# Performance work log

Hardware: AMD Instinct MI355X
Metric: run time of the kernel (lower is better)

The kernel has to match this reference:

```python
import jax, jax.numpy as jnp
import numpy as np

N_NODES = 50000
N_EDGES = 800000
N_NODE_DICT = 10000
N_EDGE_DICT = 100
EMB = 128
HID = 32
HEADS = 4
SLOPE = 0.2
LN_EPS = 1e-5


def layer_norm(x, gamma, beta):
    mu = jnp.mean(x, axis=-1, keepdims=True)
    var = jnp.mean(jnp.square(x - mu), axis=-1, keepdims=True)
    return (x - mu) * jax.lax.rsqrt(var + LN_EPS) * gamma + beta


def setup_inputs() -> dict:
    key = jax.random.key(0)
    ks = jax.random.split(key, 10)
    D = HID * HEADS
    inp = {
        "node_features": jax.random.randint(ks[0], (N_NODES,), 0, N_NODE_DICT),
        "edge_features": jax.random.randint(ks[1], (N_EDGES,), 0, N_EDGE_DICT),
        "edge_index": jax.random.randint(ks[2], (2, N_EDGES), 0, N_NODES),
        "node_emb": jax.random.normal(ks[3], (N_NODE_DICT, EMB), jnp.float32),
        "edge_emb": jax.random.normal(ks[4], (N_EDGE_DICT, EMB), jnp.float32),
        "w_W": jax.random.normal(ks[5], (EMB, D), jnp.float32) / np.sqrt(EMB),
        "w_b": jnp.zeros((D,), jnp.float32),
        "ew_W": jax.random.normal(ks[6], (EMB, D), jnp.float32) / np.sqrt(EMB),
        "ew_b": jnp.zeros((D,), jnp.float32),
        "attn": jax.random.normal(ks[7], (HEADS, 3 * HID), jnp.float32) * 0.1,
        "ln_gamma": jnp.ones((D,), jnp.float32),
        "ln_beta": jnp.zeros((D,), jnp.float32),
    }
    return inp


def reference(node_features, edge_features, edge_index, node_emb, edge_emb,
              w_W, w_b, ew_W, ew_b, attn, ln_gamma, ln_beta):
    # embedding lookups
    nf = node_emb[node_features]                       # [N, EMB]
    ef = edge_emb[edge_features]                       # [E, EMB]
    # linear projections -> [*, heads, hid]
    h = (nf @ w_W + w_b).reshape(-1, HEADS, HID)       # [N, H, F]
    eh = (ef @ ew_W + ew_b).reshape(-1, HEADS, HID)    # [E, H, F]
    tgt = edge_index[0]
    src = edge_index[1]
    # attn = [a_i || a_j || a_e]; dot with concat == sum of per-part dots
    a_i, a_j, a_e = attn[:, :HID], attn[:, HID:2 * HID], attn[:, 2 * HID:]
    s_i = jnp.einsum('nhf,hf->nh', h, a_i)             # [N, H]
    s_j = jnp.einsum('nhf,hf->nh', h, a_j)             # [N, H]
    s_e = jnp.einsum('ehf,hf->eh', eh, a_e)            # [E, H]
    eij = jax.nn.leaky_relu(s_i[tgt] + s_j[src] + s_e, negative_slope=SLOPE)  # [E, H]
    # scatter softmax over edges grouped by target node
    m = jax.ops.segment_max(eij, tgt, num_segments=N_NODES)   # [N, H]
    ex = jnp.exp(eij - m[tgt])
    denom = jax.ops.segment_sum(ex, tgt, num_segments=N_NODES)
    alpha = ex / denom[tgt]                            # [E, H]
    # message passing + scatter_add
    message = alpha[..., None] * h[src]                # [E, H, F]
    out = jax.ops.segment_sum(message, tgt, num_segments=N_NODES)  # [N, H, F]
    out = out + h                                      # skip connection
    out = out.reshape(-1, HEADS * HID)                 # concat heads
    eh2 = eh.reshape(-1, HEADS * HID)
    out = layer_norm(out, ln_gamma, ln_beta)
    eh2 = layer_norm(eh2, ln_gamma, ln_beta)
    return out, eh2
```

## Files before the change

### kernel.cpp

```cpp
#include <hip/hip_runtime.h>

#define NNODES 50000
#define NEDGES 800000
#define NNODE_DICT 10000
#define NEDGE_DICT 100
#define EMB 128
#define HID 32
#define HEADS 4
#define DD 128
#define SLOPE 0.2f
#define LN_EPS 1e-5f
#define NEG_BIG -3.0e38f

#define NDICT_BLOCKS (NNODE_DICT / 4)
#define EDICT_BLOCKS (NEDGE_DICT)
#define COUNT_BLOCKS ((NEDGES / 4 + 127) / 128)
#define NTILES ((NNODES + 1023) / 1024)
#define AGG_BLOCKS ((NNODES + 3) / 4)
#define EOUT_BLOCKS (NEDGES * 32 / 256)
#define BACK_BLOCKS (AGG_BLOCKS + EOUT_BLOCKS)

typedef float vfloat4 __attribute__((ext_vector_type(4)));

__global__ __launch_bounds__(128) void front_kernel(
        const float* __restrict__ node_emb,
        const float* __restrict__ w_W,
        const float* __restrict__ w_b,
        const float* __restrict__ attn,
        float* __restrict__ h_dict,
        float* __restrict__ s_i_d,
        float* __restrict__ s_j_d,
        const float* __restrict__ edge_emb,
        const float* __restrict__ ew_W,
        const float* __restrict__ ew_b,
        const float* __restrict__ gamma,
        const float* __restrict__ beta,
        float* __restrict__ eh2_dict,
        float* __restrict__ s_e_d,
        const int* __restrict__ edge_index,
        int* __restrict__ counts) {
    __shared__ float a_sh[4][EMB];
    __shared__ float red[4];
    int bid = blockIdx.x;
    int col = threadIdx.x;

    if (bid < NDICT_BLOCKS) {
        int r0 = bid * 4;
        #pragma unroll
        for (int r = 0; r < 4; ++r) a_sh[r][col] = node_emb[(r0 + r) * EMB + col];
        __syncthreads();
        float acc0 = 0.f, acc1 = 0.f, acc2 = 0.f, acc3 = 0.f;
        #pragma unroll 8
        for (int k = 0; k < EMB; ++k) {
            float wv = w_W[k * DD + col];
            acc0 += a_sh[0][k] * wv;
            acc1 += a_sh[1][k] * wv;
            acc2 += a_sh[2][k] * wv;
            acc3 += a_sh[3][k] * wv;
        }
        float b = w_b[col];
        acc0 += b; acc1 += b; acc2 += b; acc3 += b;
        h_dict[(r0 + 0) * DD + col] = acc0;
        h_dict[(r0 + 1) * DD + col] = acc1;
        h_dict[(r0 + 2) * DD + col] = acc2;
        h_dict[(r0 + 3) * DD + col] = acc3;

        int head = col >> 5, f = col & 31;
        float ai = attn[head * 96 + f];
        float aj = attn[head * 96 + 32 + f];
        float accs[4] = {acc0, acc1, acc2, acc3};
        #pragma unroll
        for (int r = 0; r < 4; ++r) {
            float pi = accs[r] * ai;
            float pj = accs[r] * aj;
            #pragma unroll
            for (int off = 16; off > 0; off >>= 1) {
                pi += __shfl_down(pi, off);
                pj += __shfl_down(pj, off);
            }
            if ((col & 31) == 0) {
                s_i_d[(r0 + r) * HEADS + head] = pi;
                s_j_d[(r0 + r) * HEADS + head] = pj;
            }
        }
    } else if (bid < NDICT_BLOCKS + EDICT_BLOCKS) {
        int row = bid - NDICT_BLOCKS;
        a_sh[0][col] = edge_emb[row * EMB + col];
        __syncthreads();
        float acc = 0.f;
        #pragma unroll 8
        for (int k = 0; k < EMB; ++k) acc += a_sh[0][k] * ew_W[k * DD + col];
        acc += ew_b[col];

        int head = col >> 5, f = col & 31;
        float pe = acc * attn[head * 96 + 64 + f];
        #pragma unroll
        for (int off = 16; off > 0; off >>= 1) pe += __shfl_down(pe, off);
        if ((col & 31) == 0) s_e_d[row * HEADS + head] = pe;

        float s = acc, s2 = acc * acc;
        #pragma unroll
        for (int off = 32; off > 0; off >>= 1) {
            s  += __shfl_down(s, off);
            s2 += __shfl_down(s2, off);
        }
        int wid = col >> 6;
        if ((col & 63) == 0) { red[wid * 2] = s; red[wid * 2 + 1] = s2; }
        __syncthreads();
        s = red[0] + red[2];
        s2 = red[1] + red[3];
        float mu = s * (1.f / DD);
        float var = s2 * (1.f / DD) - mu * mu;
        float r = rsqrtf(var + LN_EPS);
        eh2_dict[row * DD + col] = (acc - mu) * r * gamma[col] + beta[col];
    } else {
        int i = (bid - NDICT_BLOCKS - EDICT_BLOCKS) * 128 + col;
        if (i < NEDGES / 4) {
            int4 t = ((const int4*)edge_index)[i];
            atomicAdd(&counts[t.x], 1);
            atomicAdd(&counts[t.y], 1);
            atomicAdd(&counts[t.z], 1);
            atomicAdd(&counts[t.w], 1);
        }
    }
}

__global__ __launch_bounds__(256) void scan_tiles(const int* __restrict__ counts,
                                                  int* __restrict__ excl,
                                                  int* __restrict__ tsums) {
    __shared__ int wred[4];
    int tile = blockIdx.x;
    int tid = threadIdx.x;
    int base = tile * 1024 + tid * 4;
    int4 v = make_int4(0, 0, 0, 0);
    if (base + 3 < NNODES) {
        v = *(const int4*)(counts + base);
    } else {
        if (base + 0 < NNODES) v.x = counts[base + 0];
        if (base + 1 < NNODES) v.y = counts[base + 1];
        if (base + 2 < NNODES) v.z = counts[base + 2];
        if (base + 3 < NNODES) v.w = counts[base + 3];
    }
    int tsum = v.x + v.y + v.z + v.w;
    int lane = tid & 63, w = tid >> 6;
    int incl = tsum;
    #pragma unroll
    for (int o = 1; o < 64; o <<= 1) {
        int t = __shfl_up(incl, o);
        if (lane >= o) incl += t;
    }
    if (lane == 63) wred[w] = incl;
    __syncthreads();
    int wexc = 0;
    #pragma unroll
    for (int j = 0; j < 4; ++j) if (j < w) wexc += wred[j];
    int ex = wexc + incl - tsum;
    int4 o4 = make_int4(ex, ex + v.x, ex + v.x + v.y, ex + v.x + v.y + v.z);
    if (base + 3 < NNODES) {
        *(int4*)(excl + base) = o4;
    } else {
        if (base + 0 < NNODES) excl[base + 0] = o4.x;
        if (base + 1 < NNODES) excl[base + 1] = o4.y;
        if (base + 2 < NNODES) excl[base + 2] = o4.z;
        if (base + 3 < NNODES) excl[base + 3] = o4.w;
    }
    if (tid == 255) tsums[tile] = wexc + incl;
}

__global__ __launch_bounds__(256) void scan_fixup2(const int* __restrict__ tsums,
                                                   int* __restrict__ offsets,
                                                   int* __restrict__ cursor) {
    __shared__ int sbase[64];
    int tid = threadIdx.x;
    if (tid < 64) {
        int v = (tid < NTILES) ? tsums[tid] : 0;
        int incl = v;
        #pragma unroll
        for (int o = 1; o < 64; o <<= 1) {
            int t = __shfl_up(incl, o);
            if (tid >= o) incl += t;
        }
        sbase[tid] = incl - v;
    }
    __syncthreads();
    int i = blockIdx.x * 256 + tid;
    if (i < NNODES) {
        int v = offsets[i] + sbase[i >> 10];
        offsets[i] = v;
        cursor[i] = v;
    }
    if (blockIdx.x == 0 && tid == 0) offsets[NNODES] = NEDGES;
}

__global__ void scatter_kernel(const int* __restrict__ edge_index,
                               const int* __restrict__ node_features,
                               const int* __restrict__ edge_features,
                               int* __restrict__ cursor,
                               int2* __restrict__ csr) {
    int e = blockIdx.x * blockDim.x + threadIdx.x;
    if (e >= NEDGES) return;
    int tgt = edge_index[e];
    int src = edge_index[NEDGES + e];
    int ns = node_features[src];
    int ee = edge_features[e];
    int pos = atomicAdd(&cursor[tgt], 1);
    csr[pos] = make_int2(ns, ee);
}

__global__ __launch_bounds__(256) void back_kernel(
        const int* __restrict__ offsets,
        const int2* __restrict__ csr,
        const int* __restrict__ node_features,
        const float4* __restrict__ s_i4,
        const float4* __restrict__ s_j4,
        const float4* __restrict__ s_e4,
        const float* __restrict__ h_dict,
        const float* __restrict__ gamma,
        const float* __restrict__ beta,
        float* __restrict__ out,
        const int* __restrict__ edge_features,
        const vfloat4* __restrict__ eh2_dict4,
        vfloat4* __restrict__ out4) {
    __shared__ float sp[4][256];
    __shared__ int   sns[4][64];
    int bid = blockIdx.x;
    int a = bid / 9;
    int r9 = bid - a * 9;

    if (r9 != 0) {
        int eb = 8 * a + r9 - 1;
        int t = eb * 256 + threadIdx.x;
        int e = t >> 5;
        int j = t & 31;
        int ee = edge_features[e];
        vfloat4 v = eh2_dict4[ee * 32 + j];
        __builtin_nontemporal_store(v, out4 + (size_t)t);
        return;
    }

    int wid = threadIdx.x >> 6;
    int lane = threadIdx.x & 63;
    int n = a * 4 + wid;
    if (n >= NNODES) return;

    int nt = node_features[n];
    float4 si = s_i4[nt];
    int off = offsets[n];
    int deg = offsets[n + 1] - off;

    float m0 = NEG_BIG, m1 = NEG_BIG, m2 = NEG_BIG, m3 = NEG_BIG;
    float l0 = 0.f, l1 = 0.f, l2 = 0.f, l3 = 0.f;
    float acc0 = 0.f, acc1 = 0.f;
    int h0 = lane >> 5;
    int h1 = 2 + (lane >> 5);

    for (int base = 0; base < deg; base += 64) {
        int cnt = min(deg - base, 64);
        float4 ev = make_float4(NEG_BIG, NEG_BIG, NEG_BIG, NEG_BIG);
        int ns = 0;
        if (lane < cnt) {
            int2 pr = csr[off + base + lane];
            ns = pr.x;
            float4 sj = s_j4[pr.x];
            float4 se = s_e4[pr.y];
            ev.x = si.x + sj.x + se.x; ev.x = ev.x > 0.f ? ev.x : SLOPE * ev.x;
            ev.y = si.y + sj.y + se.y; ev.y = ev.y > 0.f ? ev.y : SLOPE * ev.y;
            ev.z = si.z + sj.z + se.z; ev.z = ev.z > 0.f ? ev.z : SLOPE * ev.z;
            ev.w = si.w + sj.w + se.w; ev.w = ev.w > 0.f ? ev.w : SLOPE * ev.w;
        }
        float4 mv = ev;
        #pragma unroll
        for (int o = 32; o > 0; o >>= 1) {
            mv.x = fmaxf(mv.x, __shfl_xor(mv.x, o));
            mv.y = fmaxf(mv.y, __shfl_xor(mv.y, o));
            mv.z = fmaxf(mv.z, __shfl_xor(mv.z, o));
            mv.w = fmaxf(mv.w, __shfl_xor(mv.w, o));
        }
        float nm0 = fmaxf(m0, mv.x), nm1 = fmaxf(m1, mv.y);
        float nm2 = fmaxf(m2, mv.z), nm3 = fmaxf(m3, mv.w);
        float4 p = make_float4(0.f, 0.f, 0.f, 0.f);
        if (lane < cnt) {
            p.x = __expf(ev.x - nm0);
            p.y = __expf(ev.y - nm1);
            p.z = __expf(ev.z - nm2);
            p.w = __expf(ev.w - nm3);
        }
        float4 sv = p;
        #pragma unroll
        for (int o = 32; o > 0; o >>= 1) {
            sv.x += __shfl_xor(sv.x, o);
            sv.y += __shfl_xor(sv.y, o);
            sv.z += __shfl_xor(sv.z, o);
            sv.w += __shfl_xor(sv.w, o);
        }
        float sc0 = __expf(m0 - nm0), sc1 = __expf(m1 - nm1);
        float sc2 = __expf(m2 - nm2), sc3 = __expf(m3 - nm3);
        l0 = l0 * sc0 + sv.x; l1 = l1 * sc1 + sv.y;
        l2 = l2 * sc2 + sv.z; l3 = l3 * sc3 + sv.w;
        m0 = nm0; m1 = nm1; m2 = nm2; m3 = nm3;
        acc0 *= (lane < 32) ? sc0 : sc1;
        acc1 *= (lane < 32) ? sc2 : sc3;
        if (lane < cnt) {
            sp[wid][lane * 4 + 0] = p.x;
            sp[wid][lane * 4 + 1] = p.y;
            sp[wid][lane * 4 + 2] = p.z;
            sp[wid][lane * 4 + 3] = p.w;
            sns[wid][lane] = ns;
        }
        int nst = sns[wid][0];
        for (int t = 0; t < cnt; ++t) {
            const float* hr = h_dict + (size_t)nst * DD;
            float w0 = sp[wid][t * 4 + h0];
            float w1 = sp[wid][t * 4 + h1];
            if (t + 1 < cnt) nst = sns[wid][t + 1];
            acc0 += w0 * hr[lane];
            acc1 += w1 * hr[lane + 64];
        }
    }

    float den0 = (lane < 32) ? l0 : l1;
    float den1 = (lane < 32) ? l2 : l3;
    float msg0 = den0 > 0.f ? acc0 / den0 : 0.f;
    float msg1 = den1 > 0.f ? acc1 / den1 : 0.f;
    const float* hres = h_dict + (size_t)nt * DD;
    float v0 = msg0 + hres[lane];
    float v1 = msg1 + hres[lane + 64];
    float s = v0 + v1, s2 = v0 * v0 + v1 * v1;
    #pragma unroll
    for (int o = 32; o > 0; o >>= 1) {
        s  += __shfl_xor(s, o);
        s2 += __shfl_xor(s2, o);
    }
    float mu = s * (1.f / DD);
    float var = s2 * (1.f / DD) - mu * mu;
    float r = rsqrtf(var + LN_EPS);
    out[(size_t)n * DD + lane]      = (v0 - mu) * r * gamma[lane] + beta[lane];
    out[(size_t)n * DD + lane + 64] = (v1 - mu) * r * gamma[lane + 64] + beta[lane + 64];
}

extern "C" void kernel_launch(void* const* d_in, const int* in_sizes, int n_in,
                              void* d_out, int out_size, void* d_ws, size_t ws_size,
                              hipStream_t stream) {
    const int*   node_features = (const int*)d_in[0];
    const int*   edge_features = (const int*)d_in[1];
    const int*   edge_index    = (const int*)d_in[2];
    const float* node_emb      = (const float*)d_in[3];
    const float* edge_emb      = (const float*)d_in[4];
    const float* w_W           = (const float*)d_in[5];
    const float* w_b           = (const float*)d_in[6];
    const float* ew_W          = (const float*)d_in[7];
    const float* ew_b          = (const float*)d_in[8];
    const float* attn          = (const float*)d_in[9];
    const float* gamma         = (const float*)d_in[10];
    const float* beta          = (const float*)d_in[11];

    float* out_nodes = (float*)d_out;
    float* out_edges = (float*)d_out + (size_t)NNODES * DD;

    char* w = (char*)d_ws;
    float* h_dict   = (float*)w;  w += (size_t)NNODE_DICT * DD * 4;
    float* s_i_d    = (float*)w;  w += (size_t)NNODE_DICT * 4 * 4;
    float* s_j_d    = (float*)w;  w += (size_t)NNODE_DICT * 4 * 4;
    float* eh2_dict = (float*)w;  w += (size_t)NEDGE_DICT * DD * 4;
    float* s_e_d    = (float*)w;  w += (size_t)NEDGE_DICT * 4 * 4;
    int*   counts   = (int*)w;    w += (size_t)NNODES * 4;
    int*   offsets  = (int*)w;    w += (size_t)(NNODES + 4) * 4;
    int*   cursor   = (int*)w;    w += (size_t)NNODES * 4;
    int*   tsums    = (int*)w;    w += (size_t)64 * 4;
    int2*  csr      = (int2*)w;   w += (size_t)NEDGES * 8;

    (void)hipMemsetAsync(counts, 0, (size_t)NNODES * 4, stream);

    front_kernel<<<NDICT_BLOCKS + EDICT_BLOCKS + COUNT_BLOCKS, 128, 0, stream>>>(
        node_emb, w_W, w_b, attn, h_dict, s_i_d, s_j_d,
        edge_emb, ew_W, ew_b, gamma, beta, eh2_dict, s_e_d,
        edge_index, counts);
    scan_tiles<<<NTILES, 256, 0, stream>>>(counts, offsets, tsums);
    scan_fixup2<<<(NNODES + 255) / 256, 256, 0, stream>>>(tsums, offsets, cursor);
    scatter_kernel<<<(NEDGES + 255) / 256, 256, 0, stream>>>(edge_index, node_features,
                                                             edge_features, cursor, csr);
    back_kernel<<<BACK_BLOCKS, 256, 0, stream>>>(offsets, csr, node_features,
                                                 (const float4*)s_i_d,
                                                 (const float4*)s_j_d,
                                                 (const float4*)s_e_d,
                                                 h_dict, gamma, beta, out_nodes,
                                                 edge_features,
                                                 (const vfloat4*)eh2_dict,
                                                 (vfloat4*)out_edges);
}
```

Measured before the change: 584.6 us.

## Fuse all stages into one persistent kernel with grid barriers and spread edge output

Replaces the five kernel launches and the memset with a single persistent kernel of 2048 blocks that uses atomic grid barriers between phases. The streaming edge-output gather is split across all phases so it fills the idle blocks during the small scan and fixup stages. Counts are zeroed inside the kernel. This removes launch gaps and tail underutilisation, at the cost of grid barrier latency and a dependence on all 2048 blocks being co-resident, which could deadlock if they are not.

```diff
diff --git a/kernel.cpp b/kernel.cpp
--- a/kernel.cpp
+++ b/kernel.cpp
@@ -12,330 +12,368 @@
 #define LN_EPS 1e-5f
 #define NEG_BIG -3.0e38f
 
-#define NDICT_BLOCKS (NNODE_DICT / 4)
-#define EDICT_BLOCKS (NEDGE_DICT)
-#define COUNT_BLOCKS ((NEDGES / 4 + 127) / 128)
+#define G 2048
+
+#define NGEMM_N 2500
+#define NGEMM_E 100
+#define W_P0 (NGEMM_N + NGEMM_E)
+#define CNT_BEQ 1563
 #define NTILES ((NNODES + 1023) / 1024)
-#define AGG_BLOCKS ((NNODES + 3) / 4)
-#define EOUT_BLOCKS (NEDGES * 32 / 256)
-#define BACK_BLOCKS (AGG_BLOCKS + EOUT_BLOCKS)
+#define FIX_BEQ ((NNODES + 127) / 128)
+#define SCAT_BEQ (NEDGES / 128)
+#define AGG_BEQ (NNODES / 2)
+#define EOUT_BEQ 200000
+#define E1 50000
+#define E2 12500
+#define E3 12500
+#define E4 50000
+#define E5 75000
 
 typedef float vfloat4 __attribute__((ext_vector_type(4)));
 
-__global__ __launch_bounds__(128) void front_kernel(
+__device__ __forceinline__ void gridbar(unsigned int* bar, unsigned int target) {
+    __syncthreads();
+    if (threadIdx.x == 0) {
+        __hip_atomic_fetch_add(bar, 1u, __ATOMIC_ACQ_REL, __HIP_MEMORY_SCOPE_AGENT);
+        unsigned int v;
+        do {
+            __builtin_amdgcn_s_sleep(2);
+            v = __hip_atomic_load(bar, __ATOMIC_ACQUIRE, __HIP_MEMORY_SCOPE_AGENT);
+        } while (v < target);
+    }
+    __syncthreads();
+}
+
+__global__ __launch_bounds__(128, 4) void mega_kernel(
+        const int* __restrict__ node_features,
+        const int* __restrict__ edge_features,
+        const int* __restrict__ edge_index,
         const float* __restrict__ node_emb,
+        const float* __restrict__ edge_emb,
         const float* __restrict__ w_W,
         const float* __restrict__ w_b,
+        const float* __restrict__ ew_W,
+        const float* __restrict__ ew_b,
         const float* __restrict__ attn,
+        const float* __restrict__ gamma,
+        const float* __restrict__ beta,
         float* __restrict__ h_dict,
         float* __restrict__ s_i_d,
         float* __restrict__ s_j_d,
-        const float* __restrict__ edge_emb,
-        const float* __restrict__ ew_W,
-        const float* __restrict__ ew_b,
-        const float* __restrict__ gamma,
-        const float* __restrict__ beta,
         float* __restrict__ eh2_dict,
         float* __restrict__ s_e_d,
-        const int* __restrict__ edge_index,
-        int* __restrict__ counts) {
+        int* __restrict__ counts,
+        int* __restrict__ offsets,
+        int* __restrict__ cursor,
+        int* __restrict__ tsums,
+        int2* __restrict__ csr,
+        float* __restrict__ out_nodes,
+        vfloat4* __restrict__ out_edges4,
+        unsigned int* __restrict__ bar) {
     __shared__ float a_sh[4][EMB];
-    __shared__ float red[4];
-    int bid = blockIdx.x;
-    int col = threadIdx.x;
-
-    if (bid < NDICT_BLOCKS) {
-        int r0 = bid * 4;
+    __shared__ float redp[4];
+    __shared__ int   wred[2];
+    __shared__ int   sbase[64];
+    __shared__ float sp[2][256];
+    __shared__ int   sns[2][64];
+
+    const int bid = blockIdx.x;
+    const int tid = threadIdx.x;
+    const vfloat4* eh2_dict4 = (const vfloat4*)eh2_dict;
+
+    {
+        int i = bid * 128 + tid;
+        if (i < NNODES) counts[i] = 0;
+    }
+    for (int w = bid; w < W_P0; w += G) {
+        if (w < NGEMM_N) {
+            int r0 = w * 4;
+            #pragma unroll
+            for (int r = 0; r < 4; ++r) a_sh[r][tid] = node_emb[(r0 + r) * EMB + tid];
+            __syncthreads();
+            float acc0 = 0.f, acc1 = 0.f, acc2 = 0.f, acc3 = 0.f;
+            #pragma unroll 8
+            for (int k = 0; k < EMB; ++k) {
+                float wv = w_W[k * DD + tid];
+                acc0 += a_sh[0][k] * wv;
+                acc1 += a_sh[1][k] * wv;
+                acc2 += a_sh[2][k] * wv;
+                acc3 += a_sh[3][k] * wv;
+            }
+            float b = w_b[tid];
+            acc0 += b; acc1 += b; acc2 += b; acc3 += b;
+            h_dict[(r0 + 0) * DD + tid] = acc0;
+            h_dict[(r0 + 1) * DD + tid] = acc1;
+            h_dict[(r0 + 2) * DD + tid] = acc2;
+            h_dict[(r0 + 3) * DD + tid] = acc3;
+
+            int head = tid >> 5, f = tid & 31;
+            float ai = attn[head * 96 + f];
+            float aj = attn[head * 96 + 32 + f];
+            float accs[4] = {acc0, acc1, acc2, acc3};
+            #pragma unroll
+            for (int r = 0; r < 4; ++r) {
+                float pi = accs[r] * ai;
+                float pj = accs[r] * aj;
+                #pragma unroll
+                for (int off = 16; off > 0; off >>= 1) {
+                    pi += __shfl_down(pi, off);
+                    pj += __shfl_down(pj, off);
+                }
+                if ((tid & 31) == 0) {
+                    s_i_d[(r0 + r) * HEADS + head] = pi;
+                    s_j_d[(r0 + r) * HEADS + head] = pj;
+                }
+            }
+            __syncthreads();
+        } else {
+            int row = w - NGEMM_N;
+            a_sh[0][tid] = edge_emb[row * EMB + tid];
+            __syncthreads();
+            float acc = 0.f;
+            #pragma unroll 8
+            for (int k = 0; k < EMB; ++k) acc += a_sh[0][k] * ew_W[k * DD + tid];
+            acc += ew_b[tid];
+
+            int head = tid >> 5, f = tid & 31;
+            float pe = acc * attn[head * 96 + 64 + f];
+            #pragma unroll
+            for (int off = 16; off > 0; off >>= 1) pe += __shfl_down(pe, off);
+            if ((tid & 31) == 0) s_e_d[row * HEADS + head] = pe;
+
+            float s = acc, s2 = acc * acc;
+            #pragma unroll
+            for (int off = 32; off > 0; off >>= 1) {
+                s  += __shfl_down(s, off);
+                s2 += __shfl_down(s2, off);
+            }
+            int wv = tid >> 6;
+            if ((tid & 63) == 0) { redp[wv * 2] = s; redp[wv * 2 + 1] = s2; }
+            __syncthreads();
+            s  = redp[0] + redp[2];
+            s2 = redp[1] + redp[3];
+            float mu = s * (1.f / DD);
+            float var = s2 * (1.f / DD) - mu * mu;
+            float rr = rsqrtf(var + LN_EPS);
+            eh2_dict[row * DD + tid] = (acc - mu) * rr * gamma[tid] + beta[tid];
+            __syncthreads();
+        }
+    }
+    gridbar(bar, 1u * G);
+
+    for (int w = bid; w < CNT_BEQ + E1; w += G) {
+        if (w < CNT_BEQ) {
+            int i = w * 128 + tid;
+            if (i < NEDGES / 4) {
+                int4 t = ((const int4*)edge_index)[i];
+                atomicAdd(&counts[t.x], 1);
+                atomicAdd(&counts[t.y], 1);
+                atomicAdd(&counts[t.z], 1);
+                atomicAdd(&counts[t.w], 1);
+            }
+        } else {
+            int q = w - CNT_BEQ;
+            int t = q * 128 + tid;
+            int e = t >> 5, j = t & 31;
+            int ee = edge_features[e];
+            __builtin_nontemporal_store(eh2_dict4[ee * 32 + j], out_edges4 + (size_t)t);
+        }
+    }
+    gridbar(bar, 2u * G);
+
+    for (int w = bid; w < NTILES + E2; w += G) {
+        if (w < NTILES) {
+            int base = w * 1024 + tid * 8;
+            int v[8]; int s8 = 0;
+            #pragma unroll
+            for (int k = 0; k < 8; ++k) {
+                int c = (base + k < NNODES) ? counts[base + k] : 0;
+                v[k] = c; s8 += c;
+            }
+            int lane = tid & 63, wv = tid >> 6;
+            int incl = s8;
+            #pragma unroll
+            for (int o = 1; o < 64; o <<= 1) {
+                int t = __shfl_up(incl, o);
+                if (lane >= o) incl += t;
+            }
+            if (lane == 63) wred[wv] = incl;
+            __syncthreads();
+            int wbase = (wv == 1) ? wred[0] : 0;
+            int ex = wbase + incl - s8;
+            #pragma unroll
+            for (int k = 0; k < 8; ++k) {
+                if (base + k < NNODES) offsets[base + k] = ex;
+                ex += v[k];
+            }
+            if (tid == 127) tsums[w] = wred[0] + incl;
+        } else {
+            int q = E1 + (w - NTILES);
+            int t = q * 128 + tid;
+            int e = t >> 5, j = t & 31;
+            int ee = edge_features[e];
+            __builtin_nontemporal_store(eh2_dict4[ee * 32 + j], out_edges4 + (size_t)t);
+        }
+    }
+    gridbar(bar, 3u * G);
+
+    for (int w = bid; w < FIX_BEQ + E3; w += G) {
+        if (w < FIX_BEQ) {
+            if (tid < 64) {
+                int vv = (tid < NTILES) ? tsums[tid] : 0;
+                int incl = vv;
+                #pragma unroll
+                for (int o = 1; o < 64; o <<= 1) {
+                    int t = __shfl_up(incl, o);
+                    if (tid >= o) incl += t;
+                }
+                sbase[tid] = incl - vv;
+            }
+            __syncthreads();
+            int i = w * 128 + tid;
+            if (i < NNODES) {
+                int vo = offsets[i] + sbase[i >> 10];
+                offsets[i] = vo;
+                cursor[i] = vo;
+            }
+            if (w == 0 && tid == 0) offsets[NNODES] = NEDGES;
+            __syncthreads();
+        } else {
+            int q = E1 + E2 + (w - FIX_BEQ);
+            int t = q * 128 + tid;
+            int e = t >> 5, j = t & 31;
+            int ee = edge_features[e];
+            __builtin_nontemporal_store(eh2_dict4[ee * 32 + j], out_edges4 + (size_t)t);
+        }
+    }
+    gridbar(bar, 4u * G);
+
+    for (int w = bid; w < SCAT_BEQ + E4; w += G) {
+        if (w < SCAT_BEQ) {
+            int e = w * 128 + tid;
+            int tgt = edge_index[e];
+            int src = edge_index[NEDGES + e];
+            int ns = node_features[src];
+            int ee = edge_features[e];
+            int pos = atomicAdd(&cursor[tgt], 1);
+            csr[pos] = make_int2(ns, ee);
+        } else {
+            int q = E1 + E2 + E3 + (w - SCAT_BEQ);
+            int t = q * 128 + tid;
+            int e = t >> 5, j = t & 31;
+            int ee = edge_features[e];
+            __builtin_nontemporal_store(eh2_dict4[ee * 32 + j], out_edges4 + (size_t)t);
+        }
+    }
+    gridbar(bar, 5u * G);
+
+    for (int w = bid; w < AGG_BEQ + E5; w += G) {
+        if (w >= AGG_BEQ) {
+            int q = E1 + E2 + E3 + E4 + (w - AGG_BEQ);
+            int t = q * 128 + tid;
+            int e = t >> 5, j = t & 31;
+            int ee = edge_features[e];
+            __builtin_nontemporal_store(eh2_dict4[ee * 32 + j], out_edges4 + (size_t)t);
+            continue;
+        }
+        int wid = tid >> 6;
+        int lane = tid & 63;
+        int n = w * 2 + wid;
+
+        int nt = node_features[n];
+        float4 si = ((const float4*)s_i_d)[nt];
+        int off = offsets[n];
+        int deg = offsets[n + 1] - off;
+
+        float m0 = NEG_BIG, m1 = NEG_BIG, m2 = NEG_BIG, m3 = NEG_BIG;
+        float l0 = 0.f, l1 = 0.f, l2 = 0.f, l3 = 0.f;
+        float acc0 = 0.f, acc1 = 0.f;
+        int h0 = lane >> 5;
+        int h1 = 2 + (lane >> 5);
+
+        for (int base = 0; base < deg; base += 64) {
+            int cnt = min(deg - base, 64);
+            float4 ev = make_float4(NEG_BIG, NEG_BIG, NEG_BIG, NEG_BIG);
+            int ns = 0;
+            if (lane < cnt) {
+                int2 pr = csr[off + base + lane];
+                ns = pr.x;
+                float4 sj = ((const float4*)s_j_d)[pr.x];
+                float4 se = ((const float4*)s_e_d)[pr.y];
+                ev.x = si.x + sj.x + se.x; ev.x = ev.x > 0.f ? ev.x : SLOPE * ev.x;
+                ev.y = si.y + sj.y + se.y; ev.y = ev.y > 0.f ? ev.y : SLOPE * ev.y;
+                ev.z = si.z + sj.z + se.z; ev.z = ev.z > 0.f ? ev.z : SLOPE * ev.z;
+                ev.w = si.w + sj.w + se.w; ev.w = ev.w > 0.f ? ev.w : SLOPE * ev.w;
+            }
+            float4 mv = ev;
+            #pragma unroll
+            for (int o = 32; o > 0; o >>= 1) {
+                mv.x = fmaxf(mv.x, __shfl_xor(mv.x, o));
+                mv.y = fmaxf(mv.y, __shfl_xor(mv.y, o));
+                mv.z = fmaxf(mv.z, __shfl_xor(mv.z, o));
+                mv.w = fmaxf(mv.w, __shfl_xor(mv.w, o));
+            }
+            float nm0 = fmaxf(m0, mv.x), nm1 = fmaxf(m1, mv.y);
+            float nm2 = fmaxf(m2, mv.z), nm3 = fmaxf(m3, mv.w);
+            float4 p = make_float4(0.f, 0.f, 0.f, 0.f);
+            if (lane < cnt) {
+                p.x = __expf(ev.x - nm0);
+                p.y = __expf(ev.y - nm1);
+                p.z = __expf(ev.z - nm2);
+                p.w = __expf(ev.w - nm3);
+            }
+            float4 sv = p;
+            #pragma unroll
+            for (int o = 32; o > 0; o >>= 1) {
+                sv.x += __shfl_xor(sv.x, o);
+                sv.y += __shfl_xor(sv.y, o);
+                sv.z += __shfl_xor(sv.z, o);
+                sv.w += __shfl_xor(sv.w, o);
+            }
+            float sc0 = __expf(m0 - nm0), sc1 = __expf(m1 - nm1);
+            float sc2 = __expf(m2 - nm2), sc3 = __expf(m3 - nm3);
+            l0 = l0 * sc0 + sv.x; l1 = l1 * sc1 + sv.y;
+            l2 = l2 * sc2 + sv.z; l3 = l3 * sc3 + sv.w;
+            m0 = nm0; m1 = nm1; m2 = nm2; m3 = nm3;
+            acc0 *= (lane < 32) ? sc0 : sc1;
+            acc1 *= (lane < 32) ? sc2 : sc3;
+            if (lane < cnt) {
+                sp[wid][lane * 4 + 0] = p.x;
+                sp[wid][lane * 4 + 1] = p.y;
+                sp[wid][lane * 4 + 2] = p.z;
+                sp[wid][lane * 4 + 3] = p.w;
+                sns[wid][lane] = ns;
+            }
+            int nst = sns[wid][0];
+            for (int t = 0; t < cnt; ++t) {
+                const float* hr = h_dict + (size_t)nst * DD;
+                float w0 = sp[wid][t * 4 + h0];
+                float w1 = sp[wid][t * 4 + h1];
+                if (t + 1 < cnt) nst = sns[wid][t + 1];
+                acc0 += w0 * hr[lane];
+                acc1 += w1 * hr[lane + 64];
+            }
+        }
+
+        float den0 = (lane < 32) ? l0 : l1;
+        float den1 = (lane < 32) ? l2 : l3;
+        float msg0 = den0 > 0.f ? acc0 / den0 : 0.f;
+        float msg1 = den1 > 0.f ? acc1 / den1 : 0.f;
+        const float* hres = h_dict + (size_t)nt * DD;
+        float v0 = msg0 + hres[lane];
+        float v1 = msg1 + hres[lane + 64];
+        float s = v0 + v1, s2 = v0 * v0 + v1 * v1;
         #pragma unroll
-        for (int r = 0; r < 4; ++r) a_sh[r][col] = node_emb[(r0 + r) * EMB + col];
-        __syncthreads();
-        float acc0 = 0.f, acc1 = 0.f, acc2 = 0.f, acc3 = 0.f;
-        #pragma unroll 8
-        for (int k = 0; k < EMB; ++k) {
-            float wv = w_W[k * DD + col];
-            acc0 += a_sh[0][k] * wv;
-            acc1 += a_sh[1][k] * wv;
-            acc2 += a_sh[2][k] * wv;
-            acc3 += a_sh[3][k] * wv;
-        }
-        float b = w_b[col];
-        acc0 += b; acc1 += b; acc2 += b; acc3 += b;
-        h_dict[(r0 + 0) * DD + col] = acc0;
-        h_dict[(r0 + 1) * DD + col] = acc1;
-        h_dict[(r0 + 2) * DD + col] = acc2;
-        h_dict[(r0 + 3) * DD + col] = acc3;
-
-        int head = col >> 5, f = col & 31;
-        float ai = attn[head * 96 + f];
-        float aj = attn[head * 96 + 32 + f];
-        float accs[4] = {acc0, acc1, acc2, acc3};
-        #pragma unroll
-        for (int r = 0; r < 4; ++r) {
-            float pi = accs[r] * ai;
-            float pj = accs[r] * aj;
-            #pragma unroll
-            for (int off = 16; off > 0; off >>= 1) {
-                pi += __shfl_down(pi, off);
-                pj += __shfl_down(pj, off);
-            }
-            if ((col & 31) == 0) {
-                s_i_d[(r0 + r) * HEADS + head] = pi;
-                s_j_d[(r0 + r) * HEADS + head] = pj;
-            }
-        }
-    } else if (bid < NDICT_BLOCKS + EDICT_BLOCKS) {
-        int row = bid - NDICT_BLOCKS;
-        a_sh[0][col] = edge_emb[row * EMB + col];
-        __syncthreads();
-        float acc = 0.f;
-        #pragma unroll 8
-        for (int k = 0; k < EMB; ++k) acc += a_sh[0][k] * ew_W[k * DD + col];
-        acc += ew_b[col];
-
-        int head = col >> 5, f = col & 31;
-        float pe = acc * attn[head * 96 + 64 + f];
-        #pragma unroll
-        for (int off = 16; off > 0; off >>= 1) pe += __shfl_down(pe, off);
-        if ((col & 31) == 0) s_e_d[row * HEADS + head] = pe;
-
-        float s = acc, s2 = acc * acc;
-        #pragma unroll
-        for (int off = 32; off > 0; off >>= 1) {
-            s  += __shfl_down(s, off);
-            s2 += __shfl_down(s2, off);
-        }
-        int wid = col >> 6;
-        if ((col & 63) == 0) { red[wid * 2] = s; red[wid * 2 + 1] = s2; }
-        __syncthreads();
-        s = red[0] + red[2];
-        s2 = red[1] + red[3];
+        for (int o = 32; o > 0; o >>= 1) {
+            s  += __shfl_xor(s, o);
+            s2 += __shfl_xor(s2, o);
+        }
         float mu = s * (1.f / DD);
         float var = s2 * (1.f / DD) - mu * mu;
-        float r = rsqrtf(var + LN_EPS);
-        eh2_dict[row * DD + col] = (acc - mu) * r * gamma[col] + beta[col];
-    } else {
-        int i = (bid - NDICT_BLOCKS - EDICT_BLOCKS) * 128 + col;
-        if (i < NEDGES / 4) {
-            int4 t = ((const int4*)edge_index)[i];
-            atomicAdd(&counts[t.x], 1);
-            atomicAdd(&counts[t.y], 1);
-            atomicAdd(&counts[t.z], 1);
-            atomicAdd(&counts[t.w], 1);
-        }
-    }
-}
-
-__global__ __launch_bounds__(256) void scan_tiles(const int* __restrict__ counts,
-                                                  int* __restrict__ excl,
-                                                  int* __restrict__ tsums) {
-    __shared__ int wred[4];
-    int tile = blockIdx.x;
-    int tid = threadIdx.x;
-    int base = tile * 1024 + tid * 4;
-    int4 v = make_int4(0, 0, 0, 0);
-    if (base + 3 < NNODES) {
-        v = *(const int4*)(counts + base);
-    } else {
-        if (base + 0 < NNODES) v.x = counts[base + 0];
-        if (base + 1 < NNODES) v.y = counts[base + 1];
-        if (base + 2 < NNODES) v.z = counts[base + 2];
-        if (base + 3 < NNODES) v.w = counts[base + 3];
-    }
-    int tsum = v.x + v.y + v.z + v.w;
-    int lane = tid & 63, w = tid >> 6;
-    int incl = tsum;
-    #pragma unroll
-    for (int o = 1; o < 64; o <<= 1) {
-        int t = __shfl_up(incl, o);
-        if (lane >= o) incl += t;
-    }
-    if (lane == 63) wred[w] = incl;
-    __syncthreads();
-    int wexc = 0;
-    #pragma unroll
-    for (int j = 0; j < 4; ++j) if (j < w) wexc += wred[j];
-    int ex = wexc + incl - tsum;
-    int4 o4 = make_int4(ex, ex + v.x, ex + v.x + v.y, ex + v.x + v.y + v.z);
-    if (base + 3 < NNODES) {
-        *(int4*)(excl + base) = o4;
-    } else {
-        if (base + 0 < NNODES) excl[base + 0] = o4.x;
-        if (base + 1 < NNODES) excl[base + 1] = o4.y;
-        if (base + 2 < NNODES) excl[base + 2] = o4.z;
-        if (base + 3 < NNODES) excl[base + 3] = o4.w;
-    }
-    if (tid == 255) tsums[tile] = wexc + incl;
-}
-
-__global__ __launch_bounds__(256) void scan_fixup2(const int* __restrict__ tsums,
-                                                   int* __restrict__ offsets,
-                                                   int* __restrict__ cursor) {
-    __shared__ int sbase[64];
-    int tid = threadIdx.x;
-    if (tid < 64) {
-        int v = (tid < NTILES) ? tsums[tid] : 0;
-        int incl = v;
-        #pragma unroll
-        for (int o = 1; o < 64; o <<= 1) {
-            int t = __shfl_up(incl, o);
-            if (tid >= o) incl += t;
-        }
-        sbase[tid] = incl - v;
-    }
-    __syncthreads();
-    int i = blockIdx.x * 256 + tid;
-    if (i < NNODES) {
-        int v = offsets[i] + sbase[i >> 10];
-        offsets[i] = v;
-        cursor[i] = v;
-    }
-    if (blockIdx.x == 0 && tid == 0) offsets[NNODES] = NEDGES;
-}
-
-__global__ void scatter_kernel(const int* __restrict__ edge_index,
-                               const int* __restrict__ node_features,
-                               const int* __restrict__ edge_features,
-                               int* __restrict__ cursor,
-                               int2* __restrict__ csr) {
-    int e = blockIdx.x * blockDim.x + threadIdx.x;
-    if (e >= NEDGES) return;
-    int tgt = edge_index[e];
-    int src = edge_index[NEDGES + e];
-    int ns = node_features[src];
-    int ee = edge_features[e];
-    int pos = atomicAdd(&cursor[tgt], 1);
-    csr[pos] = make_int2(ns, ee);
-}
-
-__global__ __launch_bounds__(256) void back_kernel(
-        const int* __restrict__ offsets,
-        const int2* __restrict__ csr,
-        const int* __restrict__ node_features,
-        const float4* __restrict__ s_i4,
-        const float4* __restrict__ s_j4,
-        const float4* __restrict__ s_e4,
-        const float* __restrict__ h_dict,
-        const float* __restrict__ gamma,
-        const float* __restrict__ beta,
-        float* __restrict__ out,
-        const int* __restrict__ edge_features,
-        const vfloat4* __restrict__ eh2_dict4,
-        vfloat4* __restrict__ out4) {
-    __shared__ float sp[4][256];
-    __shared__ int   sns[4][64];
-    int bid = blockIdx.x;
-    int a = bid / 9;
-    int r9 = bid - a * 9;
-
-    if (r9 != 0) {
-        int eb = 8 * a + r9 - 1;
-        int t = eb * 256 + threadIdx.x;
-        int e = t >> 5;
-        int j = t & 31;
-        int ee = edge_features[e];
-        vfloat4 v = eh2_dict4[ee * 32 + j];
-        __builtin_nontemporal_store(v, out4 + (size_t)t);
-        return;
-    }
-
-    int wid = threadIdx.x >> 6;
-    int lane = threadIdx.x & 63;
-    int n = a * 4 + wid;
-    if (n >= NNODES) return;
-
-    int nt = node_features[n];
-    float4 si = s_i4[nt];
-    int off = offsets[n];
-    int deg = offsets[n + 1] - off;
-
-    float m0 = NEG_BIG, m1 = NEG_BIG, m2 = NEG_BIG, m3 = NEG_BIG;
-    float l0 = 0.f, l1 = 0.f, l2 = 0.f, l3 = 0.f;
-    float acc0 = 0.f, acc1 = 0.f;
-    int h0 = lane >> 5;
-    int h1 = 2 + (lane >> 5);
-
-    for (int base = 0; base < deg; base += 64) {
-        int cnt = min(deg - base, 64);
-        float4 ev = make_float4(NEG_BIG, NEG_BIG, NEG_BIG, NEG_BIG);
-        int ns = 0;
-        if (lane < cnt) {
-            int2 pr = csr[off + base + lane];
-            ns = pr.x;
-            float4 sj = s_j4[pr.x];
-            float4 se = s_e4[pr.y];
-            ev.x = si.x + sj.x + se.x; ev.x = ev.x > 0.f ? ev.x : SLOPE * ev.x;
-            ev.y = si.y + sj.y + se.y; ev.y = ev.y > 0.f ? ev.y : SLOPE * ev.y;
-            ev.z = si.z + sj.z + se.z; ev.z = ev.z > 0.f ? ev.z : SLOPE * ev.z;
-            ev.w = si.w + sj.w + se.w; ev.w = ev.w > 0.f ? ev.w : SLOPE * ev.w;
-        }
-        float4 mv = ev;
-        #pragma unroll
-        for (int o = 32; o > 0; o >>= 1) {
-            mv.x = fmaxf(mv.x, __shfl_xor(mv.x, o));
-            mv.y = fmaxf(mv.y, __shfl_xor(mv.y, o));
-            mv.z = fmaxf(mv.z, __shfl_xor(mv.z, o));
-            mv.w = fmaxf(mv.w, __shfl_xor(mv.w, o));
-        }
-        float nm0 = fmaxf(m0, mv.x), nm1 = fmaxf(m1, mv.y);
-        float nm2 = fmaxf(m2, mv.z), nm3 = fmaxf(m3, mv.w);
-        float4 p = make_float4(0.f, 0.f, 0.f, 0.f);
-        if (lane < cnt) {
-            p.x = __expf(ev.x - nm0);
-            p.y = __expf(ev.y - nm1);
-            p.z = __expf(ev.z - nm2);
-            p.w = __expf(ev.w - nm3);
-        }
-        float4 sv = p;
-        #pragma unroll
-        for (int o = 32; o > 0; o >>= 1) {
-            sv.x += __shfl_xor(sv.x, o);
-            sv.y += __shfl_xor(sv.y, o);
-            sv.z += __shfl_xor(sv.z, o);
-            sv.w += __shfl_xor(sv.w, o);
-        }
-        float sc0 = __expf(m0 - nm0), sc1 = __expf(m1 - nm1);
-        float sc2 = __expf(m2 - nm2), sc3 = __expf(m3 - nm3);
-        l0 = l0 * sc0 + sv.x; l1 = l1 * sc1 + sv.y;
-        l2 = l2 * sc2 + sv.z; l3 = l3 * sc3 + sv.w;
-        m0 = nm0; m1 = nm1; m2 = nm2; m3 = nm3;
-        acc0 *= (lane < 32) ? sc0 : sc1;
-        acc1 *= (lane < 32) ? sc2 : sc3;
-        if (lane < cnt) {
-            sp[wid][lane * 4 + 0] = p.x;
-            sp[wid][lane * 4 + 1] = p.y;
-            sp[wid][lane * 4 + 2] = p.z;
-            sp[wid][lane * 4 + 3] = p.w;
-            sns[wid][lane] = ns;
-        }
-        int nst = sns[wid][0];
-        for (int t = 0; t < cnt; ++t) {
-            const float* hr = h_dict + (size_t)nst * DD;
-            float w0 = sp[wid][t * 4 + h0];
-            float w1 = sp[wid][t * 4 + h1];
-            if (t + 1 < cnt) nst = sns[wid][t + 1];
-            acc0 += w0 * hr[lane];
-            acc1 += w1 * hr[lane + 64];
-        }
-    }
-
-    float den0 = (lane < 32) ? l0 : l1;
-    float den1 = (lane < 32) ? l2 : l3;
-    float msg0 = den0 > 0.f ? acc0 / den0 : 0.f;
-    float msg1 = den1 > 0.f ? acc1 / den1 : 0.f;
-    const float* hres = h_dict + (size_t)nt * DD;
-    float v0 = msg0 + hres[lane];
-    float v1 = msg1 + hres[lane + 64];
-    float s = v0 + v1, s2 = v0 * v0 + v1 * v1;
-    #pragma unroll
-    for (int o = 32; o > 0; o >>= 1) {
-        s  += __shfl_xor(s, o);
-        s2 += __shfl_xor(s2, o);
-    }
-    float mu = s * (1.f / DD);
-    float var = s2 * (1.f / DD) - mu * mu;
-    float r = rsqrtf(var + LN_EPS);
-    out[(size_t)n * DD + lane]      = (v0 - mu) * r * gamma[lane] + beta[lane];
-    out[(size_t)n * DD + lane + 64] = (v1 - mu) * r * gamma[lane + 64] + beta[lane + 64];
+        float rr = rsqrtf(var + LN_EPS);
+        out_nodes[(size_t)n * DD + lane]      = (v0 - mu) * rr * gamma[lane] + beta[lane];
+        out_nodes[(size_t)n * DD + lane + 64] = (v1 - mu) * rr * gamma[lane + 64] + beta[lane + 64];
+    }
 }
 
 extern "C" void kernel_launch(void* const* d_in, const int* in_sizes, int n_in,
@@ -368,23 +406,14 @@
     int*   cursor   = (int*)w;    w += (size_t)NNODES * 4;
     int*   tsums    = (int*)w;    w += (size_t)64 * 4;
     int2*  csr      = (int2*)w;   w += (size_t)NEDGES * 8;
-
-    (void)hipMemsetAsync(counts, 0, (size_t)NNODES * 4, stream);
-
-    front_kernel<<<NDICT_BLOCKS + EDICT_BLOCKS + COUNT_BLOCKS, 128, 0, stream>>>(
-        node_emb, w_W, w_b, attn, h_dict, s_i_d, s_j_d,
-        edge_emb, ew_W, ew_b, gamma, beta, eh2_dict, s_e_d,
-        edge_index, counts);
-    scan_tiles<<<NTILES, 256, 0, stream>>>(counts, offsets, tsums);
-    scan_fixup2<<<(NNODES + 255) / 256, 256, 0, stream>>>(tsums, offsets, cursor);
-    scatter_kernel<<<(NEDGES + 255) / 256, 256, 0, stream>>>(edge_index, node_features,
-                                                             edge_features, cursor, csr);
-    back_kernel<<<BACK_BLOCKS, 256, 0, stream>>>(offsets, csr, node_features,
-                                                 (const float4*)s_i_d,
-                                                 (const float4*)s_j_d,
-                                                 (const float4*)s_e_d,
-                                                 h_dict, gamma, beta, out_nodes,
-                                                 edge_features,
-                                                 (const vfloat4*)eh2_dict,
-                                                 (vfloat4*)out_edges);
+    unsigned int* bar = (unsigned int*)w; w += 16;
+
+    (void)hipMemsetAsync(bar, 0, 16, stream);
+
+    mega_kernel<<<G, 128, 0, stream>>>(
+        node_features, edge_features, edge_index,
+        node_emb, edge_emb, w_W, w_b, ew_W, ew_b, attn, gamma, beta,
+        h_dict, s_i_d, s_j_d, eh2_dict, s_e_d,
+        counts, offsets, cursor, tsums, csr,
+        out_nodes, (vfloat4*)out_edges, bar);
 }
```

Result: slower. 1.722 ms (+194.5%).

## Spread edge-output gather stores across count, scatter and back kernels

Applied to the files above, without the earlier changes.

Splits the 410 MB edge-output gather/store work (eh2 per edge) into three slices, piggybacked onto the count, scatter and back kernels, instead of doing it all inside back_kernel. Counting moves out of front_kernel into a new kernel that runs after the dictionary projections, so eh2_dict is ready. The aim is to overlap bandwidth-bound output stores with the latency-bound atomic count and scatter phases. The cost is one extra kernel launch, and the store traffic now competes with the atomics.

```diff
diff --git a/kernel.cpp b/kernel.cpp
--- a/kernel.cpp
+++ b/kernel.cpp
@@ -14,13 +14,33 @@
 
 #define NDICT_BLOCKS (NNODE_DICT / 4)
 #define EDICT_BLOCKS (NEDGE_DICT)
-#define COUNT_BLOCKS ((NEDGES / 4 + 127) / 128)
+#define FRONT_BLOCKS (NDICT_BLOCKS + EDICT_BLOCKS)
 #define NTILES ((NNODES + 1023) / 1024)
+
+#define CNT_BLOCKS ((NEDGES / 4 + 255) / 256)
+#define EOUT_A 25000
+#define K1_BLOCKS (CNT_BLOCKS + EOUT_A)
+
+#define SCAT_BLOCKS (NEDGES / 256)
+#define EOUT_B 25000
+#define K4_BLOCKS (SCAT_BLOCKS + EOUT_B)
+
 #define AGG_BLOCKS ((NNODES + 3) / 4)
-#define EOUT_BLOCKS (NEDGES * 32 / 256)
-#define BACK_BLOCKS (AGG_BLOCKS + EOUT_BLOCKS)
+#define EOUT_C 50000
+#define BACK_BLOCKS (AGG_BLOCKS + EOUT_C)
 
 typedef float vfloat4 __attribute__((ext_vector_type(4)));
+
+__device__ __forceinline__ void eout_store(const int* __restrict__ edge_features,
+                                           const vfloat4* __restrict__ eh2_dict4,
+                                           vfloat4* __restrict__ out4,
+                                           int q , int tid) {
+    int t = q * 256 + tid;
+    int e = t >> 5;
+    int j = t & 31;
+    int ee = edge_features[e];
+    __builtin_nontemporal_store(eh2_dict4[ee * 32 + j], out4 + (size_t)t);
+}
 
 __global__ __launch_bounds__(128) void front_kernel(
         const float* __restrict__ node_emb,
@@ -36,9 +56,7 @@
         const float* __restrict__ gamma,
         const float* __restrict__ beta,
         float* __restrict__ eh2_dict,
-        float* __restrict__ s_e_d,
-        const int* __restrict__ edge_index,
-        int* __restrict__ counts) {
+        float* __restrict__ s_e_d) {
     __shared__ float a_sh[4][EMB];
     __shared__ float red[4];
     int bid = blockIdx.x;
@@ -83,7 +101,7 @@
                 s_j_d[(r0 + r) * HEADS + head] = pj;
             }
         }
-    } else if (bid < NDICT_BLOCKS + EDICT_BLOCKS) {
+    } else {
         int row = bid - NDICT_BLOCKS;
         a_sh[0][col] = edge_emb[row * EMB + col];
         __syncthreads();
@@ -113,8 +131,19 @@
         float var = s2 * (1.f / DD) - mu * mu;
         float r = rsqrtf(var + LN_EPS);
         eh2_dict[row * DD + col] = (acc - mu) * r * gamma[col] + beta[col];
-    } else {
-        int i = (bid - NDICT_BLOCKS - EDICT_BLOCKS) * 128 + col;
+    }
+}
+
+__global__ __launch_bounds__(256) void count_eout_kernel(
+        const int* __restrict__ edge_index,
+        int* __restrict__ counts,
+        const int* __restrict__ edge_features,
+        const vfloat4* __restrict__ eh2_dict4,
+        vfloat4* __restrict__ out4) {
+    int bid = blockIdx.x;
+    int tid = threadIdx.x;
+    if (bid < CNT_BLOCKS) {
+        int i = bid * 256 + tid;
         if (i < NEDGES / 4) {
             int4 t = ((const int4*)edge_index)[i];
             atomicAdd(&counts[t.x], 1);
@@ -122,6 +151,8 @@
             atomicAdd(&counts[t.z], 1);
             atomicAdd(&counts[t.w], 1);
         }
+    } else {
+        eout_store(edge_features, eh2_dict4, out4, bid - CNT_BLOCKS, tid);
     }
 }
 
@@ -192,19 +223,28 @@
     if (blockIdx.x == 0 && tid == 0) offsets[NNODES] = NEDGES;
 }
 
-__global__ void scatter_kernel(const int* __restrict__ edge_index,
-                               const int* __restrict__ node_features,
-                               const int* __restrict__ edge_features,
-                               int* __restrict__ cursor,
-                               int2* __restrict__ csr) {
-    int e = blockIdx.x * blockDim.x + threadIdx.x;
-    if (e >= NEDGES) return;
-    int tgt = edge_index[e];
-    int src = edge_index[NEDGES + e];
-    int ns = node_features[src];
-    int ee = edge_features[e];
-    int pos = atomicAdd(&cursor[tgt], 1);
-    csr[pos] = make_int2(ns, ee);
+__global__ __launch_bounds__(256) void scatter_eout_kernel(
+        const int* __restrict__ edge_index,
+        const int* __restrict__ node_features,
+        const int* __restrict__ edge_features,
+        int* __restrict__ cursor,
+        int2* __restrict__ csr,
+        const vfloat4* __restrict__ eh2_dict4,
+        vfloat4* __restrict__ out4) {
+    int bid = blockIdx.x;
+    int tid = threadIdx.x;
+    if (bid < SCAT_BLOCKS) {
+        int e = bid * 256 + tid;
+        int tgt = edge_index[e];
+        int src = edge_index[NEDGES + e];
+        int ns = node_features[src];
+        int ee = edge_features[e];
+        int pos = atomicAdd(&cursor[tgt], 1);
+        csr[pos] = make_int2(ns, ee);
+    } else {
+        eout_store(edge_features, eh2_dict4, out4,
+                   EOUT_A + (bid - SCAT_BLOCKS), tid);
+    }
 }
 
 __global__ __launch_bounds__(256) void back_kernel(
@@ -224,17 +264,12 @@
     __shared__ float sp[4][256];
     __shared__ int   sns[4][64];
     int bid = blockIdx.x;
-    int a = bid / 9;
-    int r9 = bid - a * 9;
-
-    if (r9 != 0) {
-        int eb = 8 * a + r9 - 1;
-        int t = eb * 256 + threadIdx.x;
-        int e = t >> 5;
-        int j = t & 31;
-        int ee = edge_features[e];
-        vfloat4 v = eh2_dict4[ee * 32 + j];
-        __builtin_nontemporal_store(v, out4 + (size_t)t);
+    int a = bid / 5;
+    int r5 = bid - a * 5;
+
+    if (r5 != 0) {
+        eout_store(edge_features, eh2_dict4, out4,
+                   EOUT_A + EOUT_B + 4 * a + r5 - 1, threadIdx.x);
         return;
     }
 
@@ -371,14 +406,17 @@
 
     (void)hipMemsetAsync(counts, 0, (size_t)NNODES * 4, stream);
 
-    front_kernel<<<NDICT_BLOCKS + EDICT_BLOCKS + COUNT_BLOCKS, 128, 0, stream>>>(
+    front_kernel<<<FRONT_BLOCKS, 128, 0, stream>>>(
         node_emb, w_W, w_b, attn, h_dict, s_i_d, s_j_d,
-        edge_emb, ew_W, ew_b, gamma, beta, eh2_dict, s_e_d,
-        edge_index, counts);
+        edge_emb, ew_W, ew_b, gamma, beta, eh2_dict, s_e_d);
+    count_eout_kernel<<<K1_BLOCKS, 256, 0, stream>>>(
+        edge_index, counts, edge_features,
+        (const vfloat4*)eh2_dict, (vfloat4*)out_edges);
     scan_tiles<<<NTILES, 256, 0, stream>>>(counts, offsets, tsums);
     scan_fixup2<<<(NNODES + 255) / 256, 256, 0, stream>>>(tsums, offsets, cursor);
-    scatter_kernel<<<(NEDGES + 255) / 256, 256, 0, stream>>>(edge_index, node_features,
-                                                             edge_features, cursor, csr);
+    scatter_eout_kernel<<<K4_BLOCKS, 256, 0, stream>>>(
+        edge_index, node_features, edge_features, cursor, csr,
+        (const vfloat4*)eh2_dict, (vfloat4*)out_edges);
     back_kernel<<<BACK_BLOCKS, 256, 0, stream>>>(offsets, csr, node_features,
                                                  (const float4*)s_i_d,
                                                  (const float4*)s_j_d,
```

Result: no change. 591.3 us (+1.2%).
